# Kernel tuning notes

Measured on AMD Instinct MI355X. Metric: run time of the kernel, lower is better.

Reference implementation:

```python
import jax, jax.numpy as jnp
import numpy as np

B, S, HID, H = 4, 2048, 1024, 16
D = HID // H  # dim per head


def setup_inputs() -> dict:
    key = jax.random.key(0)
    ks = jax.random.split(key, 7)
    inp = {
        "q": jax.random.normal(ks[0], (B, S, HID), dtype=jnp.float32),
        "k": jax.random.normal(ks[1], (B, S, HID), dtype=jnp.float32),
        "v": jax.random.normal(ks[2], (B, S, HID), dtype=jnp.float32),
        # Linear weights stored as (in, out); applied as x @ W. use_bias=False.
        "Wq": jax.random.normal(ks[3], (HID, HID), dtype=jnp.float32) * (1.0 / np.sqrt(HID)),
        "Wk": jax.random.normal(ks[4], (HID, HID), dtype=jnp.float32) * (1.0 / np.sqrt(HID)),
        "Wv": jax.random.normal(ks[5], (HID, HID), dtype=jnp.float32) * (1.0 / np.sqrt(HID)),
        "Wo": jax.random.normal(ks[6], (HID, HID), dtype=jnp.float32) * (1.0 / np.sqrt(HID)),
    }
    return inp


def reference(q, k, v, Wq, Wk, Wv, Wo):
    scale = 1.0 / jnp.sqrt(jnp.float32(D))
    # QKV projections, then split hidden into (H, D) heads (same layout as transpose_qkv)
    Q = (q @ Wq).reshape(B, S, H, D)
    K = (k @ Wk).reshape(B, S, H, D)
    V = (v @ Wv).reshape(B, S, H, D)
    # scaled dot-product attention: full [B,H,S,S] score matrix, softmax over keys
    attn_w = jnp.einsum("bqhd,bkhd->bhqk", Q, K) * scale
    attn_w = jax.nn.softmax(attn_w, axis=-1)
    # dropout rate is 0 (eval-mode / deterministic)
    O = jnp.einsum("bhqk,bkhd->bqhd", attn_w, V).reshape(B, S, HID)
    return O @ Wo
```

## Files before the change

### kernel.cpp

```cpp
#include <hip/hip_runtime.h>


typedef __attribute__((ext_vector_type(8))) short short8;
typedef __attribute__((ext_vector_type(4))) float float4v;
typedef __attribute__((ext_vector_type(16))) float float16v;
typedef __attribute__((ext_vector_type(2))) unsigned int uint2v;

#if __has_builtin(__builtin_amdgcn_exp2f)
#define EXP2F(x) __builtin_amdgcn_exp2f(x)
#else
#define EXP2F(x) exp2f(x)
#endif

__device__ __forceinline__ unsigned short f2b(float x) {
  return (unsigned short)((__float_as_uint(x) + 0x8000u) >> 16);
}
__device__ __forceinline__ unsigned pk2f(float a, float b) {
  unsigned ua = __float_as_uint(a) + 0x8000u;
  unsigned ub = __float_as_uint(b) + 0x8000u;
  return __builtin_amdgcn_perm(ub, ua, 0x07060302);
}

typedef __attribute__((address_space(3))) unsigned int lds_uint;
typedef const __attribute__((address_space(1))) unsigned int gbl_uint;
__device__ __forceinline__ void stage16(const unsigned short* g, unsigned short* l) {
#if __has_builtin(__builtin_amdgcn_global_load_lds)
  __builtin_amdgcn_global_load_lds((gbl_uint*)g, (lds_uint*)l, 16, 0, 0);
#else
  *(uint4*)l = *(const uint4*)g;
#endif
}

__global__ __launch_bounds__(256) void conv_qkv(const float* __restrict__ q,
                                                const float* __restrict__ k,
                                                const float* __restrict__ v,
                                                unsigned short* __restrict__ ws,
                                                float qscale) {
  const int z = blockIdx.y;
  const float* src = z == 0 ? q : (z == 1 ? k : v);
  unsigned short* dst = ws + (size_t)z * 8388608;
  const float s = z == 0 ? qscale : 1.0f;
  size_t i = ((size_t)blockIdx.x * 256 + threadIdx.x) * 8;
  float4v a = *(const float4v*)(src + i);
  float4v b = *(const float4v*)(src + i + 4);
  uint4 o;
  o.x = pk2f(a.x * s, a.y * s);
  o.y = pk2f(a.z * s, a.w * s);
  o.z = pk2f(b.x * s, b.y * s);
  o.w = pk2f(b.z * s, b.w * s);
  *(uint4*)(dst + i) = o;
}

__global__ __launch_bounds__(256) void wtrans(const float* __restrict__ Wq,
                                              const float* __restrict__ Wk,
                                              const float* __restrict__ Wv,
                                              const float* __restrict__ Wo,
                                              unsigned short* __restrict__ Wt) {
  __shared__ float tile[32][33];
  const float* W = blockIdx.z == 0 ? Wq : blockIdx.z == 1 ? Wk
                   : blockIdx.z == 2 ? Wv : Wo;
  unsigned short* T = Wt + (size_t)blockIdx.z * 1048576;
  const int tx = threadIdx.x & 31, ty = threadIdx.x >> 5;
  const int k0 = blockIdx.y * 32, n0 = blockIdx.x * 32;
#pragma unroll
  for (int i = 0; i < 4; i++)
    tile[ty + 8 * i][tx] = W[(size_t)(k0 + ty + 8 * i) * 1024 + n0 + tx];
  __syncthreads();
#pragma unroll
  for (int i = 0; i < 4; i++)
    T[(size_t)(n0 + ty + 8 * i) * 1024 + k0 + tx] = f2b(tile[tx][ty + 8 * i]);
}

template <int MODE, bool SWAP>
__global__ __launch_bounds__(256, 2) void gemm_bt(const unsigned short* __restrict__ A,
                                                  const unsigned short* __restrict__ Bt,
                                                  void* __restrict__ Cg) {
  __shared__ __align__(16) unsigned short As[128 * 64];
  __shared__ __align__(16) unsigned short Bs[128 * 64];
  const int tid = threadIdx.x;
  const int lane = tid & 63;
  const int w = tid >> 6;
  const int quad = lane >> 4, col = lane & 15;
  const int wm = w >> 1, wn = w & 1;
  const int lin = blockIdx.x;
  const int xcd = lin & 7, grp = lin >> 3;
  const int m0 = ((grp & 7) * 8 + xcd) * 128;
  const int n0 = (grp >> 3) * 128;
  const int rA = lane >> 3, cA = lane & 7;

  float4v acc[4][4] = {};

  for (int k0 = 0; k0 < 1024; k0 += 64) {
    __syncthreads();
#pragma unroll
    for (int j = 0; j < 4; j++) {
      const int row = w * 32 + j * 8 + rA;
      stage16(A + (unsigned)(m0 + row) * 1024 + k0 + ((cA ^ rA) * 8),
              &As[row * 64 + cA * 8]);
      stage16(Bt + (unsigned)(n0 + row) * 1024 + k0 + ((cA ^ rA) * 8),
              &Bs[row * 64 + cA * 8]);
    }
    __syncthreads();

#pragma unroll
    for (int ks = 0; ks < 2; ks++) {
      short8 af[4], bf[4];
#pragma unroll
      for (int mi = 0; mi < 4; mi++) {
        int row = wm * 64 + mi * 16 + col;
        af[mi] = *(const short8*)&As[row * 64 + (((ks * 4 + quad) ^ (col & 7)) * 8)];
      }
#pragma unroll
      for (int ni = 0; ni < 4; ni++) {
        int row = wn * 64 + ni * 16 + col;
        bf[ni] = *(const short8*)&Bs[row * 64 + (((ks * 4 + quad) ^ (col & 7)) * 8)];
      }
#pragma unroll
      for (int mi = 0; mi < 4; mi++)
#pragma unroll
        for (int ni = 0; ni < 4; ni++) {
          if (SWAP)
            acc[ni][mi] = __builtin_amdgcn_mfma_f32_16x16x32_bf16(
                bf[ni], af[mi], acc[ni][mi], 0, 0, 0);
          else
            acc[mi][ni] = __builtin_amdgcn_mfma_f32_16x16x32_bf16(
                af[mi], bf[ni], acc[mi][ni], 0, 0, 0);
        }
    }
  }

  if (MODE == 0) {
#pragma unroll
    for (int ni = 0; ni < 4; ni++) {
      const int cg = n0 + wn * 64 + ni * 16 + quad * 4;
      const int h = cg >> 6, dlo = cg & 63;
#pragma unroll
      for (int mi = 0; mi < 4; mi++) {
        const int tok = m0 + wm * 64 + mi * 16 + col;
        const int b = tok >> 11, s = tok & 2047;
        uint2 pk;
        pk.x = pk2f(acc[ni][mi][0], acc[ni][mi][1]);
        pk.y = pk2f(acc[ni][mi][2], acc[ni][mi][3]);
        *(uint2*)((unsigned short*)Cg +
                  ((unsigned)((b * 16 + h) * 2048 + s) * 64 + dlo)) = pk;
      }
    }
  } else if (MODE == 1) {
#pragma unroll
    for (int mi = 0; mi < 4; mi++) {
      const int tok = m0 + wm * 64 + mi * 16 + quad * 4;
      const int b = tok >> 11, s = tok & 2047;
#pragma unroll
      for (int ni = 0; ni < 4; ni++) {
        const int cg = n0 + wn * 64 + ni * 16 + col;
        const int h = cg >> 6, d = cg & 63;
        uint2 pk;
        pk.x = pk2f(acc[mi][ni][0], acc[mi][ni][1]);
        pk.y = pk2f(acc[mi][ni][2], acc[mi][ni][3]);
        *(uint2*)((unsigned short*)Cg +
                  ((unsigned)((b * 16 + h) * 64 + d) * 2048 + s)) = pk;
      }
    }
  } else {
#pragma unroll
    for (int mi = 0; mi < 4; mi++) {
      const int row = m0 + wm * 64 + mi * 16 + quad * 4;
#pragma unroll
      for (int ni = 0; ni < 4; ni++) {
        const int cg = n0 + wn * 64 + ni * 16 + col;
#pragma unroll
        for (int r = 0; r < 4; r++)
          ((float*)Cg)[(unsigned)(row + r) * 1024 + cg] = acc[mi][ni][r];
      }
    }
  }
}

__global__ __launch_bounds__(256, 2) void attn_kernel(
    const unsigned short* __restrict__ Qb, const unsigned short* __restrict__ Kb,
    const unsigned short* __restrict__ Vt, unsigned short* __restrict__ Ob) {
  __shared__ __align__(16) unsigned short K_lds[2][64 * 64];
  __shared__ __align__(16) unsigned short V_lds[2][64 * 64];

  const int tid = threadIdx.x;
  const int lane = tid & 63;
  const int w = tid >> 6;
  const int l5 = lane & 31, hi = lane >> 5;

  const int lin = blockIdx.x;
  const int bh = ((lin >> 3) & 7) * 8 + (lin & 7);
  const int qt = lin >> 6;

  const unsigned short* Kbase = Kb + (size_t)bh * (2048 * 64);
  const unsigned short* Vbase = Vt + (size_t)bh * (64 * 2048);
  const int q0 = qt * 128 + w * 32;

  short8 qf[4];
#pragma unroll
  for (int c = 0; c < 4; c++)
    qf[c] = *(const short8*)(Qb + ((size_t)bh * 2048 + q0 + l5) * 64 + c * 16 + hi * 8);

  float16v oacc[2] = {};
  float denp[4] = {};

  const int sr = lane >> 3, sc = lane & 7;

  auto STAGE = [&](int b, int kt) {
    const int s0 = kt * 64;
#pragma unroll
    for (int j = 0; j < 2; j++) {
      const int row = w * 16 + j * 8 + sr;
      stage16(Kbase + (unsigned)(s0 + row) * 64 + ((sc ^ sr) * 8),
              &K_lds[b][row * 64 + sc * 8]);
      stage16(Vbase + (unsigned)row * 2048 + s0 + ((sc ^ sr) * 8),
              &V_lds[b][row * 64 + sc * 8]);
    }
  };

  STAGE(0, 0);
  __syncthreads();

  int cur = 0;
  for (int kt = 0; kt < 32; kt++) {
    if (kt < 31) STAGE(cur ^ 1, kt + 1);

    const unsigned short* Kl = &K_lds[cur][0];
    const unsigned short* Vl = &V_lds[cur][0];

    float16v sacc[2] = {};
    __builtin_amdgcn_s_setprio(1);
#pragma unroll
    for (int t = 0; t < 2; t++)
#pragma unroll
      for (int c = 0; c < 4; c++) {
        short8 kf = *(const short8*)&Kl[(t * 32 + l5) * 64 +
                                        (((c * 2 + hi) ^ (l5 & 7)) * 8)];
        sacc[t] = __builtin_amdgcn_mfma_f32_32x32x16_bf16(kf, qf[c], sacc[t], 0, 0, 0);
      }
    __builtin_amdgcn_s_setprio(0);

    short8 pf[4];
#pragma unroll
    for (int t = 0; t < 2; t++) {
#pragma unroll
      for (int r = 0; r < 16; r++) {
        float p = EXP2F(sacc[t][r]);
        sacc[t][r] = p;
        denp[r & 3] += p;
      }
#pragma unroll
      for (int half = 0; half < 2; half++) {
        const int k0 = half * 8;
        unsigned P0 = pk2f(sacc[t][k0 + 0], sacc[t][k0 + 1]);
        unsigned P1 = pk2f(sacc[t][k0 + 2], sacc[t][k0 + 3]);
        unsigned P2 = pk2f(sacc[t][k0 + 4], sacc[t][k0 + 5]);
        unsigned P3 = pk2f(sacc[t][k0 + 6], sacc[t][k0 + 7]);
        unsigned u0, u1, u2, u3;
#if __has_builtin(__builtin_amdgcn_permlane32_swap)
        uint2v a02 = __builtin_amdgcn_permlane32_swap(P0, P2, false, false);
        uint2v a13 = __builtin_amdgcn_permlane32_swap(P1, P3, false, false);
        u0 = a02[0]; u2 = a02[1];
        u1 = a13[0]; u3 = a13[1];
#else
        unsigned p0s = __shfl_xor((int)P0, 32), p2s = __shfl_xor((int)P2, 32);
        unsigned p1s = __shfl_xor((int)P1, 32), p3s = __shfl_xor((int)P3, 32);
        u0 = hi ? p2s : P0; u2 = hi ? P2 : p0s;
        u1 = hi ? p3s : P1; u3 = hi ? P3 : p1s;
#endif
        union { unsigned u[4]; short8 s; } cv;
        cv.u[0] = u0; cv.u[1] = u1; cv.u[2] = u2; cv.u[3] = u3;
        pf[t * 2 + half] = cv.s;
      }
    }

    __builtin_amdgcn_s_setprio(1);
#pragma unroll
    for (int dt = 0; dt < 2; dt++)
#pragma unroll
      for (int kc = 0; kc < 4; kc++) {
        short8 vf = *(const short8*)&Vl[(dt * 32 + l5) * 64 +
                                        (((kc * 2 + hi) ^ (l5 & 7)) * 8)];
        oacc[dt] = __builtin_amdgcn_mfma_f32_32x32x16_bf16(vf, pf[kc], oacc[dt], 0, 0, 0);
      }
    __builtin_amdgcn_s_setprio(0);

    __syncthreads();
    cur ^= 1;
  }

  float den = (denp[0] + denp[1]) + (denp[2] + denp[3]);
  den += __shfl_xor(den, 32);
  const float rd = 1.f / den;

  const int b = bh >> 4, h = bh & 15;
  const unsigned obase = (unsigned)(b * 2048 + q0 + l5) * 1024 + h * 64;
#pragma unroll
  for (int dt = 0; dt < 2; dt++)
#pragma unroll
    for (int g = 0; g < 4; g++) {
      uint2 pk;
      pk.x = pk2f(oacc[dt][4 * g + 0] * rd, oacc[dt][4 * g + 1] * rd);
      pk.y = pk2f(oacc[dt][4 * g + 2] * rd, oacc[dt][4 * g + 3] * rd);
      *(uint2*)(Ob + obase + dt * 32 + 8 * g + 4 * hi) = pk;
    }
}

extern "C" void kernel_launch(void* const* d_in, const int* in_sizes, int n_in,
                              void* d_out, int out_size, void* d_ws, size_t ws_size,
                              hipStream_t stream) {
  const float* q = (const float*)d_in[0];
  const float* k = (const float*)d_in[1];
  const float* v = (const float*)d_in[2];
  const float* Wq = (const float*)d_in[3];
  const float* Wk = (const float*)d_in[4];
  const float* Wv = (const float*)d_in[5];
  const float* Wo = (const float*)d_in[6];

  unsigned short* ws = (unsigned short*)d_ws;
  unsigned short* qb = ws;
  unsigned short* kb = ws + 8388608;
  unsigned short* vb = ws + 16777216;
  unsigned short* Qb = ws + 25165824;
  unsigned short* Kb = ws + 33554432;
  unsigned short* Vt = ws + 41943040;
  unsigned short* Wt = ws + 50331648;

  dim3 blk(256);
  const float qscale = 0.18033688011112042f;

  conv_qkv<<<dim3(4096, 3), blk, 0, stream>>>(q, k, v, ws, qscale);
  wtrans<<<dim3(32, 32, 4), blk, 0, stream>>>(Wq, Wk, Wv, Wo, Wt);

  gemm_bt<0, true><<<dim3(512), blk, 0, stream>>>(qb, Wt + 0 * 1048576, Qb);
  gemm_bt<0, true><<<dim3(512), blk, 0, stream>>>(kb, Wt + 1 * 1048576, Kb);
  gemm_bt<1, false><<<dim3(512), blk, 0, stream>>>(vb, Wt + 2 * 1048576, Vt);

  attn_kernel<<<dim3(1024), blk, 0, stream>>>(Qb, Kb, Vt, qb );

  gemm_bt<2, false><<<dim3(512), blk, 0, stream>>>(qb , Wt + 3 * 1048576,
                                                   (float*)d_out);
}
```

Before: 341.3 us.

## Compute softmax denominator via ones-MFMA, restructure QK loop, raise occupancy

The attention kernel now computes the softmax row sums with an extra MFMA that multiplies a ones vector by the bf16 probability tiles, replacing the per-element scalar adds and the cross-lane shuffle. The QK^T loop is split per 32-key tile so only one score accumulator is live at a time, the exp is fused into packing, and launch bounds ask for 4 blocks per CU instead of 2. bf16 conversion uses the hardware v_cvt_pk_bf16_f32 instruction. The risks are the extra MFMA work per tile, register spills under the tighter bound, and a denominator now summed from rounded bf16 probabilities.

Result: no change. 343.1 us (+0.5%).

```diff
diff --git a/kernel.cpp b/kernel.cpp
--- a/kernel.cpp
+++ b/kernel.cpp
@@ -19,6 +19,11 @@
   unsigned ua = __float_as_uint(a) + 0x8000u;
   unsigned ub = __float_as_uint(b) + 0x8000u;
   return __builtin_amdgcn_perm(ub, ua, 0x07060302);
+}
+__device__ __forceinline__ unsigned cvtpk(float a, float b) {
+  unsigned r;
+  asm("v_cvt_pk_bf16_f32 %0, %1, %2" : "=v"(r) : "v"(a), "v"(b));
+  return r;
 }
 
 typedef __attribute__((address_space(3))) unsigned int lds_uint;
@@ -176,7 +181,7 @@
   }
 }
 
-__global__ __launch_bounds__(256, 2) void attn_kernel(
+__global__ __launch_bounds__(256, 4) void attn_kernel(
     const unsigned short* __restrict__ Qb, const unsigned short* __restrict__ Kb,
     const unsigned short* __restrict__ Vt, unsigned short* __restrict__ Ob) {
   __shared__ __align__(16) unsigned short K_lds[2][64 * 64];
@@ -200,8 +205,12 @@
   for (int c = 0; c < 4; c++)
     qf[c] = *(const short8*)(Qb + ((size_t)bh * 2048 + q0 + l5) * 64 + c * 16 + hi * 8);
 
+  short8 onef;
+#pragma unroll
+  for (int j = 0; j < 8; j++) onef[j] = (short)0x3F80;
+
   float16v oacc[2] = {};
-  float denp[4] = {};
+  float16v dacc = {};
 
   const int sr = lane >> 3, sc = lane & 7;
 
@@ -227,34 +236,26 @@
     const unsigned short* Kl = &K_lds[cur][0];
     const unsigned short* Vl = &V_lds[cur][0];
 
-    float16v sacc[2] = {};
-    __builtin_amdgcn_s_setprio(1);
-#pragma unroll
-    for (int t = 0; t < 2; t++)
+    short8 pf[4];
+#pragma unroll
+    for (int t = 0; t < 2; t++) {
+      float16v sacc = {};
+      __builtin_amdgcn_s_setprio(1);
 #pragma unroll
       for (int c = 0; c < 4; c++) {
         short8 kf = *(const short8*)&Kl[(t * 32 + l5) * 64 +
                                         (((c * 2 + hi) ^ (l5 & 7)) * 8)];
-        sacc[t] = __builtin_amdgcn_mfma_f32_32x32x16_bf16(kf, qf[c], sacc[t], 0, 0, 0);
-      }
-    __builtin_amdgcn_s_setprio(0);
-
-    short8 pf[4];
-#pragma unroll
-    for (int t = 0; t < 2; t++) {
-#pragma unroll
-      for (int r = 0; r < 16; r++) {
-        float p = EXP2F(sacc[t][r]);
-        sacc[t][r] = p;
-        denp[r & 3] += p;
-      }
+        sacc = __builtin_amdgcn_mfma_f32_32x32x16_bf16(kf, qf[c], sacc, 0, 0, 0);
+      }
+      __builtin_amdgcn_s_setprio(0);
+
 #pragma unroll
       for (int half = 0; half < 2; half++) {
         const int k0 = half * 8;
-        unsigned P0 = pk2f(sacc[t][k0 + 0], sacc[t][k0 + 1]);
-        unsigned P1 = pk2f(sacc[t][k0 + 2], sacc[t][k0 + 3]);
-        unsigned P2 = pk2f(sacc[t][k0 + 4], sacc[t][k0 + 5]);
-        unsigned P3 = pk2f(sacc[t][k0 + 6], sacc[t][k0 + 7]);
+        unsigned P0 = cvtpk(EXP2F(sacc[k0 + 0]), EXP2F(sacc[k0 + 1]));
+        unsigned P1 = cvtpk(EXP2F(sacc[k0 + 2]), EXP2F(sacc[k0 + 3]));
+        unsigned P2 = cvtpk(EXP2F(sacc[k0 + 4]), EXP2F(sacc[k0 + 5]));
+        unsigned P3 = cvtpk(EXP2F(sacc[k0 + 6]), EXP2F(sacc[k0 + 7]));
         unsigned u0, u1, u2, u3;
 #if __has_builtin(__builtin_amdgcn_permlane32_swap)
         uint2v a02 = __builtin_amdgcn_permlane32_swap(P0, P2, false, false);
@@ -282,15 +283,16 @@
                                         (((kc * 2 + hi) ^ (l5 & 7)) * 8)];
         oacc[dt] = __builtin_amdgcn_mfma_f32_32x32x16_bf16(vf, pf[kc], oacc[dt], 0, 0, 0);
       }
+#pragma unroll
+    for (int kc = 0; kc < 4; kc++)
+      dacc = __builtin_amdgcn_mfma_f32_32x32x16_bf16(onef, pf[kc], dacc, 0, 0, 0);
     __builtin_amdgcn_s_setprio(0);
 
     __syncthreads();
     cur ^= 1;
   }
 
-  float den = (denp[0] + denp[1]) + (denp[2] + denp[3]);
-  den += __shfl_xor(den, 32);
-  const float rd = 1.f / den;
+  const float rd = 1.f / dacc[0];
 
   const int b = bh >> 4, h = bh & 15;
   const unsigned obase = (unsigned)(b * 2048 + q0 + l5) * 1024 + h * 64;
@@ -299,8 +301,8 @@
 #pragma unroll
     for (int g = 0; g < 4; g++) {
       uint2 pk;
-      pk.x = pk2f(oacc[dt][4 * g + 0] * rd, oacc[dt][4 * g + 1] * rd);
-      pk.y = pk2f(oacc[dt][4 * g + 2] * rd, oacc[dt][4 * g + 3] * rd);
+      pk.x = cvtpk(oacc[dt][4 * g + 0] * rd, oacc[dt][4 * g + 1] * rd);
+      pk.y = cvtpk(oacc[dt][4 * g + 2] * rd, oacc[dt][4 * g + 3] * rd);
       *(uint2*)(Ob + obase + dt * 32 + 8 * g + 4 * hi) = pk;
     }
 }
```
